# Kernel tuning notes

Hardware: AMD Instinct MI355X
Metric: run time of the kernel (lower is better)

Reference implementation:

```python
import jax, jax.numpy as jnp
import numpy as np

N = 1000; K = 500; M = N - K          # codeword / info / parity bits
NUE = 4; NBS = 4                      # tx / rx antennas
BPS = 4; RATE = 0.5; NSYM = N // BPS  # 16-QAM, 250 symbols per codeword
NITER = 5                             # BP iterations

# 16-QAM constellation, Gray-coded per axis (Sionna-style), unit energy
_bits = ((np.arange(16)[:, None] >> np.array([3, 2, 1, 0])) & 1).astype(np.float32)
_re = (1 - 2 * _bits[:, 0]) * (2 - (1 - 2 * _bits[:, 2]))
_im = (1 - 2 * _bits[:, 1]) * (2 - (1 - 2 * _bits[:, 3]))
POINTS = jnp.asarray((_re + 1j * _im) / np.sqrt(10.0), dtype=jnp.complex64)  # [16]
LABELS = jnp.asarray(_bits)  # [16,4] bit labels per point


def setup_inputs() -> dict:
    key = jax.random.key(0)
    ks = jax.random.split(key, 5)
    batch = 1000
    # systematic sparse LDPC-like code: H = [P^T | I_M], info-bit degree 3
    rs = np.random.RandomState(0)
    P = np.zeros((K, M), np.int32)
    for i in range(K):
        P[i, rs.choice(M, 3, replace=False)] = 1
    vi, ci = np.nonzero(P)
    vn = np.concatenate([vi, K + np.arange(M)]).astype(np.int32)  # [2000]
    cn = np.concatenate([ci, np.arange(M)]).astype(np.int32)      # [2000]
    b = jax.random.randint(ks[0], (batch, NUE, K), 0, 2, dtype=jnp.int32)
    h_re = jax.random.normal(ks[1], (batch * NSYM, NBS, NUE), jnp.float32)
    h_im = jax.random.normal(ks[2], (batch * NSYM, NBS, NUE), jnp.float32)
    n_re = jax.random.normal(ks[3], (batch * NSYM, NBS), jnp.float32)
    n_im = jax.random.normal(ks[4], (batch * NSYM, NBS), jnp.float32)
    return {"batch_size": batch, "ebno_db": jnp.full((1,), 5.0, jnp.float32),
            "b": b, "P": jnp.asarray(P), "cn_idx": jnp.asarray(cn),
            "vn_idx": jnp.asarray(vn), "h_re": h_re, "h_im": h_im,
            "noise_re": n_re, "noise_im": n_im}


def _forward(batch_size, ebno_db, b, P, cn_idx, vn_idx, h_re, h_im, noise_re, noise_im):
    no = 1.0 / (10.0 ** (ebno_db[0] / 10.0) * BPS * RATE)  # ebnodb2no
    # --- LDPC encode (systematic): c = [b, b@P mod 2] ---
    bf = b.astype(jnp.float32)
    parity = jnp.mod(jnp.round(bf @ P.astype(jnp.float32)), 2.0)
    c = jnp.concatenate([bf, parity], -1)                    # [B,NUE,N]
    # --- QAM mapper ---
    idx = (c.reshape(batch_size, NUE, NSYM, BPS) @ jnp.array([8., 4., 2., 1.], jnp.float32)).astype(jnp.int32)
    x = POINTS[idx]                                          # [B,NUE,NSYM]
    x_f = jnp.transpose(x, (0, 2, 1)).reshape(-1, NUE)       # [B*NSYM,NUE]
    # --- flat fading channel, h ~ CN(0,1), AWGN ---
    h = ((h_re + 1j * h_im) / np.sqrt(2.0)).astype(jnp.complex64)
    w = ((noise_re + 1j * noise_im) * jnp.sqrt(no / 2.0)).astype(jnp.complex64)
    y = jnp.einsum('bij,bj->bi', h, x_f) + w                 # [B*NSYM,NBS]
    # --- LMMSE equalizer: G = H^H (H H^H + no I)^-1, unbiased scaling ---
    A = jnp.einsum('bik,bjk->bij', h, jnp.conj(h)) \
        + no.astype(jnp.complex64) * jnp.eye(NBS, dtype=jnp.complex64)
    Ainv_y = jnp.linalg.solve(A, y[..., None])[..., 0]
    x_raw = jnp.einsum('bij,bi->bj', jnp.conj(h), Ainv_y)    # G y, [B*NSYM,NUE]
    GH = jnp.einsum('bij,bik->bjk', jnp.conj(h), jnp.linalg.solve(A, h))
    d = jnp.real(jnp.diagonal(GH, axis1=1, axis2=2))         # diag(GH), [B*NSYM,NUE]
    x_hat = x_raw / d.astype(jnp.complex64)
    no_eff = jnp.maximum(1.0 / d - 1.0, 1e-12)
    x_hat = jnp.transpose(x_hat.reshape(batch_size, NSYM, NUE), (0, 2, 1))  # [B,NUE,NSYM]
    nvar = jnp.transpose(no_eff.reshape(batch_size, NSYM, NUE), (0, 2, 1))
    # --- max-log demapper, L = log p(b=0)/p(b=1) ---
    metric = -(jnp.abs(x_hat[..., None] - POINTS) ** 2) / nvar[..., None]   # [B,NUE,NSYM,16]
    NEG = jnp.float32(-1e30)
    m5 = metric[..., None, :]                               # [B,NUE,NSYM,1,16]
    lab = LABELS.T[None, None, None]                        # [1,1,1,4,16]
    m0 = jnp.max(jnp.where(lab == 0, m5, NEG), -1)
    m1 = jnp.max(jnp.where(lab == 1, m5, NEG), -1)
    llr = (m0 - m1).reshape(batch_size, NUE, N)
    # --- LDPC BP decoder (sum-product over fixed sparse Tanner graph) ---
    Lch = llr.reshape(batch_size * NUE, N).T                # [N, Bc]
    c2v = jnp.zeros((cn_idx.shape[0], Lch.shape[1]), jnp.float32)  # [E, Bc]
    for _ in range(NITER):
        vtot = Lch.at[vn_idx].add(c2v)                      # Lch + segment_sum(c2v)
        m_vc = vtot[vn_idx] - c2v                           # extrinsic VN->CN
        t = jnp.tanh(jnp.clip(m_vc * 0.5, -9.9, 9.9))
        t = jnp.where(t >= 0, jnp.maximum(t, 1e-7), jnp.minimum(t, -1e-7))
        prod = jax.ops.segment_prod(t, cn_idx, num_segments=M)
        c2v = 2.0 * jnp.arctanh(jnp.clip(prod[cn_idx] / t, -0.999999, 0.999999))
    vtot = Lch.at[vn_idx].add(c2v)
    b_hat = (vtot[:K].T < 0).astype(jnp.float32).reshape(batch_size, NUE, K)
    return bf, b_hat


def reference(batch_size, ebno_db, b, P, cn_idx, vn_idx, h_re, h_im, noise_re, noise_im):
    return _forward(batch_size, ebno_db, b, P, cn_idx, vn_idx,
                    h_re, h_im, noise_re, noise_im)
```

## Files before the change

kernel.cpp:

```cpp
#include <hip/hip_runtime.h>
#include <math.h>

#define KK     500
#define MM     500
#define NNODES 1000
#define NSYM   250
#define NITERS 5
#define MAXVDEG 4
#define EMAX   2048
#define TB     256

#define SWZ(s) ((s) ^ (((s) >> 4) & 3))

__global__ void __launch_bounds__(512)
k_setup(const int* __restrict__ cn, const int* __restrict__ vn, int E,
        const float* __restrict__ ebno, const int* __restrict__ P,
        const int* __restrict__ b, int ncw,
        int* __restrict__ cinfo, int* __restrict__ vlist, int* __restrict__ coff,
        int* __restrict__ cdend, int* __restrict__ cperm,
        double* __restrict__ nobuf, unsigned* __restrict__ Ppack,
        unsigned* __restrict__ bpack, float* __restrict__ out, int packBlocks) {
  __shared__ int sdeg[512];
  __shared__ int scinv[512];
  __shared__ int sdnew[512];
  __shared__ int sexcl[512];
  __shared__ int ssc[512];
  __shared__ int scur[512];
  __shared__ int svc[NNODES];
  __shared__ int shist[64];
  __shared__ int shcur[64];
  int tid = threadIdx.x;
  int bx = blockIdx.x;

  if (bx == 0) {
    sdeg[tid] = 0;
    for (int n = tid; n < NNODES; n += 512) svc[n] = 0;
    if (tid < 64) { shist[tid] = 0; shcur[tid] = 0; }
    __syncthreads();
    for (int e = tid; e < E; e += 512) atomicAdd(&sdeg[cn[e]], 1);
    __syncthreads();
    int d = (tid < MM) ? sdeg[tid] : 0;
    if (tid < MM) atomicAdd(&shist[d], 1);
    __syncthreads();
    if (tid == 0) {
      int acc = 0;
      for (int i = 0; i < 64; ++i) { int h = shist[i]; shist[i] = acc; shcur[i] = acc; acc += h; }
    }
    __syncthreads();
    if (tid < MM) {
      int nid = atomicAdd(&shcur[d], 1);
      scinv[tid] = nid;
      cperm[nid] = tid;
      sdnew[nid] = d;
    }
    __syncthreads();
    int v = (tid < MM) ? sdnew[tid] : 0;
    ssc[tid] = v;
    __syncthreads();
    for (int o = 1; o < 512; o <<= 1) {
      int x = (tid >= o) ? ssc[tid - o] : 0;
      __syncthreads();
      ssc[tid] += x;
      __syncthreads();
    }
    int excl = ssc[tid] - v;
    sexcl[tid] = excl;
    scur[tid] = excl;
    if (tid < MM) {
      coff[tid]  = excl;
      cdend[tid] = excl + sdnew[tid] - 1;
      if (tid == MM - 1) coff[MM] = ssc[tid];
    }
    __syncthreads();
    for (int e = tid; e < E; e += 512) {
      int c = cn[e], n = vn[e];
      int nc = scinv[c];
      int slot;
      if (n >= KK) {
        slot = sexcl[nc] + sdeg[c] - 1;
      } else {
        slot = atomicAdd(&scur[nc], 1);
      }
      cinfo[slot] = (nc << 16) | n;
      if (n < KK) {
        int t = atomicAdd(&svc[n], 1);
        if (t < MAXVDEG) vlist[n * MAXVDEG + t] = slot;
      }
    }
    if (tid == 0) {
      double no = 1.0 / (pow(10.0, (double)ebno[0] * 0.1) * 2.0);
      nobuf[0] = no;
      nobuf[1] = sqrt(no * 0.5);
    }
    return;
  }

  if (bx <= packBlocks) {
    int id = (bx - 1) * 512 + tid;
    if (id < MM * 16) {
      int j = id >> 4, w = id & 15;
      unsigned word = 0u;
      int base = w * 32;
      for (int bit = 0; bit < 32; ++bit) {
        int i = base + bit;
        if (i < KK && P[i * MM + j] != 0) word |= (1u << bit);
      }
      Ppack[j * 16 + w] = word;
    } else {
      int id2 = id - MM * 16;
      if (id2 < ncw * 16) {
        int cw = id2 >> 4, w = id2 & 15;
        unsigned word = 0u;
        int base = w * 32;
        for (int bit = 0; bit < 32; ++bit) {
          int i = base + bit;
          if (i < KK && b[cw * KK + i] != 0) word |= (1u << bit);
        }
        bpack[cw * 16 + w] = word;
      }
    }
    return;
  }

  int id = (bx - 1 - packBlocks) * 512 + tid;
  if (id < ncw * KK) out[id] = (float)b[id];
}

__device__ __forceinline__ void qam_pointf(int p, float& re, float& im) {
  const float s = 0.31622776601683794f;
  int b0 = (p >> 3) & 1, b1 = (p >> 2) & 1, b2 = (p >> 1) & 1, b3 = p & 1;
  re = (float)((1 - 2 * b0) * (2 - (1 - 2 * b2))) * s;
  im = (float)((1 - 2 * b1) * (2 - (1 - 2 * b3))) * s;
}

__device__ __forceinline__ float tanh_half(float m) {
  float mc = fminf(fmaxf(m, -19.8f), 19.8f);
  float e = __expf(mc);
  float t = 1.0f - __fdividef(2.0f, e + 1.0f);
  return (t >= 0.0f) ? fmaxf(t, 1e-7f) : fminf(t, -1e-7f);
}
__device__ __forceinline__ float pclip(float P, float t) {
  return copysignf(fminf(fabsf(P), 0.999999f * fabsf(t)), P);
}
__device__ __forceinline__ float tfloor(float t) {
  return (t >= 0.0f) ? fmaxf(t, 1e-7f) : fminf(t, -1e-7f);
}
__device__ __forceinline__ float atanh2c(float P, float t) {
  float r = __fdividef(P, t);
  r = fminf(fmaxf(r, -0.999999f), 0.999999f);
  return __logf(__fdividef(1.0f + r, 1.0f - r));
}

#define SOLVE_DEMAP(J, Lout) {                                                          \
  float u0r = Hr[0][J] * i00,               u0i = Hi[0][J] * i00;                       \
  float u1r = (Hr[1][J] - (L10r * u0r - L10i * u0i)) * i11;                             \
  float u1i = (Hi[1][J] - (L10r * u0i + L10i * u0r)) * i11;                             \
  float u2r = (Hr[2][J] - (L20r * u0r - L20i * u0i) - (L21r * u1r - L21i * u1i)) * i22; \
  float u2i = (Hi[2][J] - (L20r * u0i + L20i * u0r) - (L21r * u1i + L21i * u1r)) * i22; \
  float u3r = (Hr[3][J] - (L30r * u0r - L30i * u0i) - (L31r * u1r - L31i * u1i)         \
                        - (L32r * u2r - L32i * u2i)) * i33;                             \
  float u3i = (Hi[3][J] - (L30r * u0i + L30i * u0r) - (L31r * u1i + L31i * u1r)         \
                        - (L32r * u2i + L32i * u2r)) * i33;                             \
  float dj = (u0r * u0r + u0i * u0i) + (u1r * u1r + u1i * u1i)                          \
           + (u2r * u2r + u2i * u2i) + (u3r * u3r + u3i * u3i);                         \
  float rr = (u0r * yr[0] + u0i * yi[0]) + (u1r * yr[1] + u1i * yi[1])                  \
           + (u2r * yr[2] + u2i * yi[2]) + (u3r * yr[3] + u3i * yi[3]);                 \
  float ri = (u0r * yi[0] - u0i * yr[0]) + (u1r * yi[1] - u1i * yr[1])                  \
           + (u2r * yi[2] - u2i * yr[2]) + (u3r * yi[3] - u3i * yr[3]);                 \
  float rdj = __fdividef(1.0f, dj);                                                    \
  float xhr = rr * rdj, xhi = ri * rdj;                                                \
  float gap = 1.0f - dj;                                                               \
  float inoe = __fdividef(dj, fmaxf(gap, dj * 1e-12f));                                \
  float m0[4] = {-1e30f, -1e30f, -1e30f, -1e30f};                                      \
  float m1[4] = {-1e30f, -1e30f, -1e30f, -1e30f};                                      \
  _Pragma("unroll")                                                                    \
  for (int p = 0; p < 16; ++p) {                                                       \
    float dr = xhr - PRT[p], di = xhi - PIT[p];                                        \
    float met = -(dr * dr + di * di) * inoe;                                           \
    _Pragma("unroll")                                                                  \
    for (int k = 0; k < 4; ++k) {                                                      \
      if ((p >> (3 - k)) & 1) m1[k] = fmaxf(m1[k], met);                               \
      else                    m0[k] = fmaxf(m0[k], met);                               \
    }                                                                                  \
  }                                                                                    \
  _Pragma("unroll")                                                                    \
  for (int k = 0; k < 4; ++k) Lout[k] = m0[k] - m1[k];                                 \
}

__global__ void __launch_bounds__(256, 4)
k_fused(const float* __restrict__ h_re, const float* __restrict__ h_im,
        const float* __restrict__ n_re, const float* __restrict__ n_im,
        const double* __restrict__ nobuf,
        const unsigned* __restrict__ bpack, const unsigned* __restrict__ Ppack,
        const int* __restrict__ vlist, const int* __restrict__ coff,
        const int* __restrict__ cdend, const int* __restrict__ cperm,
        const int* __restrict__ cinfo, float* __restrict__ out, int ncw) {
  __shared__ float2 sT[EMAX];
  __shared__ float2 sP[512];
  float2* sL = sT;

  int tid = threadIdx.x;
  int pairId = blockIdx.x;
  int bt = pairId >> 1, plane = pairId & 1;

  if (tid < NSYM) {
    int t = bt * NSYM + tid;
    int s = tid;

    float no = (float)nobuf[0];
    float sq = (float)nobuf[1];
    const float is2 = 0.70710678118654752f;

    float Hr[4][4], Hi[4][4];
    {
      const float4* hr4 = (const float4*)h_re;
      const float4* hi4 = (const float4*)h_im;
      #pragma unroll
      for (int i = 0; i < 4; ++i) {
        float4 a = hr4[t * 4 + i], c = hi4[t * 4 + i];
        Hr[i][0] = a.x * is2; Hr[i][1] = a.y * is2;
        Hr[i][2] = a.z * is2; Hr[i][3] = a.w * is2;
        Hi[i][0] = c.x * is2; Hi[i][1] = c.y * is2;
        Hi[i][2] = c.z * is2; Hi[i][3] = c.w * is2;
      }
    }

    float xr[4], xi[4];
    #pragma unroll
    for (int ue = 0; ue < 4; ++ue) {
      const unsigned* bp = bpack + (bt * 4 + ue) * 16;
      int v = 0;
      #pragma unroll
      for (int k = 0; k < 4; ++k) {
        int n = 4 * s + k;
        int bit;
        if (n < KK) {
          bit = (bp[n >> 5] >> (n & 31)) & 1;
        } else {
          const unsigned* pp = Ppack + (n - KK) * 16;
          int cnt = 0;
          #pragma unroll
          for (int w = 0; w < 16; ++w) cnt += __popc(bp[w] & pp[w]);
          bit = cnt & 1;
        }
        v = (v << 1) | bit;
      }
      qam_pointf(v, xr[ue], xi[ue]);
    }

    float yr[4], yi[4];
    {
      float4 wr = ((const float4*)n_re)[t];
      float4 wi = ((const float4*)n_im)[t];
      float wrv[4] = {wr.x, wr.y, wr.z, wr.w};
      float wiv[4] = {wi.x, wi.y, wi.z, wi.w};
      #pragma unroll
      for (int i = 0; i < 4; ++i) {
        float ar = wrv[i] * sq;
        float ai = wiv[i] * sq;
        #pragma unroll
        for (int j = 0; j < 4; ++j) {
          ar += Hr[i][j] * xr[j] - Hi[i][j] * xi[j];
          ai += Hr[i][j] * xi[j] + Hi[i][j] * xr[j];
        }
        yr[i] = ar; yi[i] = ai;
      }
    }

    auto dotc = [&](int i, int j, float& ar, float& ai) {
      float r = 0.0f, m = 0.0f;
      #pragma unroll
      for (int k = 0; k < 4; ++k) {
        r += Hr[i][k] * Hr[j][k] + Hi[i][k] * Hi[j][k];
        m += Hi[i][k] * Hr[j][k] - Hr[i][k] * Hi[j][k];
      }
      ar = r; ai = m;
    };
    float a00, a11, a22, a33, dum;
    float a10r, a10i, a20r, a20i, a21r, a21i, a30r, a30i, a31r, a31i, a32r, a32i;
    dotc(0, 0, a00, dum);  a00 += no;
    dotc(1, 0, a10r, a10i);
    dotc(1, 1, a11, dum);  a11 += no;
    dotc(2, 0, a20r, a20i);
    dotc(2, 1, a21r, a21i);
    dotc(2, 2, a22, dum);  a22 += no;
    dotc(3, 0, a30r, a30i);
    dotc(3, 1, a31r, a31i);
    dotc(3, 2, a32r, a32i);
    dotc(3, 3, a33, dum);  a33 += no;

    float i00 = rsqrtf(a00);
    float L10r = a10r * i00, L10i = a10i * i00;
    float L20r = a20r * i00, L20i = a20i * i00;
    float L30r = a30r * i00, L30i = a30i * i00;
    float d11 = a11 - (L10r * L10r + L10i * L10i);
    float i11 = rsqrtf(d11);
    float L21r = (a21r - (L20r * L10r + L20i * L10i)) * i11;
    float L21i = (a21i - (L20i * L10r - L20r * L10i)) * i11;
    float L31r = (a31r - (L30r * L10r + L30i * L10i)) * i11;
    float L31i = (a31i - (L30i * L10r - L30r * L10i)) * i11;
    float d22 = a22 - (L20r * L20r + L20i * L20i) - (L21r * L21r + L21i * L21i);
    float i22 = rsqrtf(d22);
    float L32r = (a32r - (L30r * L20r + L30i * L20i) - (L31r * L21r + L31i * L21i)) * i22;
    float L32i = (a32i - (L30i * L20r - L30r * L20i) - (L31i * L21r - L31r * L21i)) * i22;
    float d33 = a33 - (L30r * L30r + L30i * L30i) - (L31r * L31r + L31i * L31i)
                    - (L32r * L32r + L32i * L32i);
    float i33 = rsqrtf(d33);

    {
      float v0r = yr[0] * i00,               v0i = yi[0] * i00;
      float v1r = (yr[1] - (L10r * v0r - L10i * v0i)) * i11;
      float v1i = (yi[1] - (L10r * v0i + L10i * v0r)) * i11;
      float v2r = (yr[2] - (L20r * v0r - L20i * v0i) - (L21r * v1r - L21i * v1i)) * i22;
      float v2i = (yi[2] - (L20r * v0i + L20i * v0r) - (L21r * v1i + L21i * v1r)) * i22;
      float v3r = (yr[3] - (L30r * v0r - L30i * v0i) - (L31r * v1r - L31i * v1i)
                         - (L32r * v2r - L32i * v2i)) * i33;
      float v3i = (yi[3] - (L30r * v0i + L30i * v0r) - (L31r * v1i + L31i * v1r)
                         - (L32r * v2i + L32i * v2r)) * i33;
      yr[0] = v0r; yi[0] = v0i; yr[1] = v1r; yi[1] = v1i;
      yr[2] = v2r; yi[2] = v2i; yr[3] = v3r; yi[3] = v3i;
    }

    const float PRT[16] = { 0.31622776601683794f, 0.31622776601683794f, 0.9486832980505138f, 0.9486832980505138f,
                            0.31622776601683794f, 0.31622776601683794f, 0.9486832980505138f, 0.9486832980505138f,
                           -0.31622776601683794f,-0.31622776601683794f,-0.9486832980505138f,-0.9486832980505138f,
                           -0.31622776601683794f,-0.31622776601683794f,-0.9486832980505138f,-0.9486832980505138f };
    const float PIT[16] = { 0.31622776601683794f, 0.9486832980505138f, 0.31622776601683794f, 0.9486832980505138f,
                           -0.31622776601683794f,-0.9486832980505138f,-0.31622776601683794f,-0.9486832980505138f,
                            0.31622776601683794f, 0.9486832980505138f, 0.31622776601683794f, 0.9486832980505138f,
                           -0.31622776601683794f,-0.9486832980505138f,-0.31622776601683794f,-0.9486832980505138f };

    float lA[4], lB[4];
    if (plane == 0) {
      SOLVE_DEMAP(0, lA);
      SOLVE_DEMAP(1, lB);
    } else {
      SOLVE_DEMAP(2, lA);
      SOLVE_DEMAP(3, lB);
    }
    #pragma unroll
    for (int k = 0; k < 4; ++k) {
      sL[4 * s + k] = make_float2(lA[k], lB[k]);
    }
  }
  __syncthreads();

  float2 Ln[2], En[2];
  int pk0[2], pk1[2], pk2[2]; bool iok[2];
  #pragma unroll
  for (int i = 0; i < 2; ++i) {
    int n = tid + TB * i;
    iok[i] = n < KK;
    Ln[i] = make_float2(0.f, 0.f);
    En[i] = make_float2(1.f, 1.f);
    pk0[i] = pk1[i] = pk2[i] = 0;
    if (iok[i]) {
      float2 L = sL[n];
      Ln[i] = L;
      En[i] = make_float2(__expf(fminf(fmaxf(L.x, -55.f), 55.f)),
                          __expf(fminf(fmaxf(L.y, -55.f), 55.f)));
      int s0 = vlist[n * MAXVDEG], s1 = vlist[n * MAXVDEG + 1], s2 = vlist[n * MAXVDEG + 2];
      pk0[i] = (cinfo[s0] & 0xffff0000) | SWZ(s0);
      pk1[i] = (cinfo[s1] & 0xffff0000) | SWZ(s1);
      pk2[i] = (cinfo[s2] & 0xffff0000) | SWZ(s2);
    }
  }
  float2 qpar0, qpar1;
  {
    int oc0 = cperm[tid];
    float2 Lp0 = sL[KK + oc0];
    qpar0 = make_float2(tanh_half(Lp0.x), tanh_half(Lp0.y));
  }
  bool c1ok = (tid + TB) < MM;
  if (c1ok) {
    int oc1 = cperm[tid + TB];
    float2 Lp1 = sL[KK + oc1];
    qpar1 = make_float2(tanh_half(Lp1.x), tanh_half(Lp1.y));
  } else {
    qpar1 = make_float2(1.f, 1.f);
  }
  int beg0 = coff[tid],                  dnd0 = cdend[tid];
  int beg1 = c1ok ? coff[tid + TB]  : 0, dnd1 = c1ok ? cdend[tid + TB] : 0;
  __syncthreads();

  for (int it = 0; it < NITERS; ++it) {
    if (it == 0) {
      #pragma unroll
      for (int i = 0; i < 2; ++i) {
        if (iok[i]) {
          float2 t = make_float2(tanh_half(Ln[i].x), tanh_half(Ln[i].y));
          sT[pk0[i] & 0xffff] = t;
          sT[pk1[i] & 0xffff] = t;
          sT[pk2[i] & 0xffff] = t;
        }
      }
    } else {
      #pragma unroll
      for (int i = 0; i < 2; ++i) {
        if (iok[i]) {
          int s0 = pk0[i] & 0xffff, c0 = ((unsigned)pk0[i]) >> 16;
          int s1 = pk1[i] & 0xffff, c1 = ((unsigned)pk1[i]) >> 16;
          int s2 = pk2[i] & 0xffff, c2 = ((unsigned)pk2[i]) >> 16;
          float2 P0 = sP[c0], P1 = sP[c1], P2 = sP[c2];
          float2 t0 = sT[s0], t1 = sT[s1], t2 = sT[s2];
          float p0 = pclip(P0.x, t0.x), p1 = pclip(P1.x, t1.x), p2 = pclip(P2.x, t2.x);
          float a0 = t0.x + p0, a1 = t1.x + p1, a2 = t2.x + p2;
          float b0 = t0.x - p0, b1 = t1.x - p1, b2 = t2.x - p2;
          float Ex = En[i].x;
          float A0 = Ex * (a1 * a2), A1 = Ex * (a0 * a2), A2 = Ex * (a0 * a1);
          float B0 = b1 * b2,        B1 = b0 * b2,        B2 = b0 * b1;
          float n0x = tfloor(__fdividef(A0 - B0, A0 + B0));
          float n1x = tfloor(__fdividef(A1 - B1, A1 + B1));
          float n2x = tfloor(__fdividef(A2 - B2, A2 + B2));
          float q0 = pclip(P0.y, t0.y), q1 = pclip(P1.y, t1.y), q2 = pclip(P2.y, t2.y);
          float c0a = t0.y + q0, c1a = t1.y + q1, c2a = t2.y + q2;
          float d0b = t0.y - q0, d1b = t1.y - q1, d2b = t2.y - q2;
          float Ey = En[i].y;
          float C0 = Ey * (c1a * c2a), C1 = Ey * (c0a * c2a), C2 = Ey * (c0a * c1a);
          float D0 = d1b * d2b,        D1 = d0b * d2b,        D2 = d0b * d1b;
          float n0y = tfloor(__fdividef(C0 - D0, C0 + D0));
          float n1y = tfloor(__fdividef(C1 - D1, C1 + D1));
          float n2y = tfloor(__fdividef(C2 - D2, C2 + D2));
          sT[s0] = make_float2(n0x, n0y);
          sT[s1] = make_float2(n1x, n1y);
          sT[s2] = make_float2(n2x, n2y);
        }
      }
    }
    __syncthreads();
    {
      float px = qpar0.x, py = qpar0.y;
      for (int e = beg0; e < dnd0; ++e) { float2 tt = sT[SWZ(e)]; px *= tt.x; py *= tt.y; }
      sP[tid] = make_float2(px, py);
      if (c1ok) {
        float qx = qpar1.x, qy = qpar1.y;
        for (int e = beg1; e < dnd1; ++e) { float2 tt = sT[SWZ(e)]; qx *= tt.x; qy *= tt.y; }
        sP[tid + TB] = make_float2(qx, qy);
      }
    }
    __syncthreads();
  }

  int cw0 = pairId * 2;
  float* o0 = out + (size_t)ncw * KK + (size_t)cw0 * KK;
  float* o1 = o0 + KK;
  #pragma unroll
  for (int i = 0; i < 2; ++i) {
    if (iok[i]) {
      int n = tid + TB * i;
      int s0 = pk0[i] & 0xffff, c0 = ((unsigned)pk0[i]) >> 16;
      int s1 = pk1[i] & 0xffff, c1 = ((unsigned)pk1[i]) >> 16;
      int s2 = pk2[i] & 0xffff, c2 = ((unsigned)pk2[i]) >> 16;
      float2 P0 = sP[c0], P1 = sP[c1], P2 = sP[c2];
      float2 t0 = sT[s0], t1 = sT[s1], t2 = sT[s2];
      float2 L = Ln[i];
      float ax = L.x + atanh2c(P0.x, t0.x) + atanh2c(P1.x, t1.x) + atanh2c(P2.x, t2.x);
      float ay = L.y + atanh2c(P0.y, t0.y) + atanh2c(P1.y, t1.y) + atanh2c(P2.y, t2.y);
      o0[n] = (ax < 0.0f) ? 1.0f : 0.0f;
      o1[n] = (ay < 0.0f) ? 1.0f : 0.0f;
    }
  }
}

extern "C" void kernel_launch(void* const* d_in, const int* in_sizes, int n_in,
                              void* d_out, int out_size, void* d_ws, size_t ws_size,
                              hipStream_t stream) {
  const float* ebno = (const float*)d_in[1];
  const int*   b    = (const int*)d_in[2];
  const int*   P    = (const int*)d_in[3];
  const int*   cn   = (const int*)d_in[4];
  const int*   vn   = (const int*)d_in[5];
  const float* h_re = (const float*)d_in[6];
  const float* h_im = (const float*)d_in[7];
  const float* nre  = (const float*)d_in[8];
  const float* nim  = (const float*)d_in[9];
  float* out = (float*)d_out;

  int E     = in_sizes[4];
  int batch = in_sizes[2] / (4 * KK);
  int ncw   = batch * 4;

  char* ws = (char*)d_ws;
  size_t off = 0;
  auto alloc = [&](size_t bytes) -> void* {
    void* p = ws + off;
    off += (bytes + 255) & ~(size_t)255;
    return p;
  };
  unsigned* Ppack  = (unsigned*)alloc((size_t)MM * 16 * 4);
  unsigned* bpack  = (unsigned*)alloc((size_t)ncw * 16 * 4);
  int*      coff   = (int*)alloc((size_t)(MM + 1) * 4);
  int*      cdend  = (int*)alloc((size_t)MM * 4);
  int*      cperm  = (int*)alloc((size_t)MM * 4);
  int*      cinfo  = (int*)alloc((size_t)EMAX * 4);
  int*      vlist  = (int*)alloc((size_t)NNODES * MAXVDEG * 4);
  double*   nobuf  = (double*)alloc(2 * 8);
  (void)ws_size; (void)n_in; (void)out_size;

  int packItems  = MM * 16 + ncw * 16;
  int packBlocks = (packItems + 511) / 512;
  int bfBlocks   = (ncw * KK + 511) / 512;
  int setupGrid  = 1 + packBlocks + bfBlocks;

  k_setup<<<dim3(setupGrid), dim3(512), 0, stream>>>(cn, vn, E, ebno, P, b, ncw,
                                                     cinfo, vlist, coff, cdend, cperm,
                                                     nobuf, Ppack, bpack, out, packBlocks);
  k_fused<<<dim3(ncw / 2), dim3(256), 0, stream>>>(h_re, h_im, nre, nim, nobuf,
                                                   bpack, Ppack, vlist, coff, cdend,
                                                   cperm, cinfo, out, ncw);
}
```

Measured before the change: 176.8 us.

## Decode all four user codewords per block instead of two

Each block now handles one batch item with all four UE codewords, vectorised as float4 in shared memory, instead of two blocks each handling two codewords. This removes the duplicated channel loading, Cholesky factorisation and index/packing work that both half-blocks previously repeated. In exchange the grid is halved, and shared memory per block and register pressure (float4 state, four demaps per thread) roughly double, which may reduce occupancy.

```diff
diff --git a/kernel.cpp b/kernel.cpp
--- a/kernel.cpp
+++ b/kernel.cpp
@@ -138,6 +138,9 @@
   float e = __expf(mc);
   float t = 1.0f - __fdividef(2.0f, e + 1.0f);
   return (t >= 0.0f) ? fmaxf(t, 1e-7f) : fminf(t, -1e-7f);
+}
+__device__ __forceinline__ float4 tanh_half4(float4 m) {
+  return make_float4(tanh_half(m.x), tanh_half(m.y), tanh_half(m.z), tanh_half(m.w));
 }
 __device__ __forceinline__ float pclip(float P, float t) {
   return copysignf(fminf(fabsf(P), 0.999999f * fabsf(t)), P);
@@ -187,6 +190,18 @@
   for (int k = 0; k < 4; ++k) Lout[k] = m0[k] - m1[k];                                 \
 }
 
+#define VUPD(C) {                                                                      \
+  float p0 = pclip(P0.C, t0.C), p1 = pclip(P1.C, t1.C), p2 = pclip(P2.C, t2.C);        \
+  float a0 = t0.C + p0, a1 = t1.C + p1, a2 = t2.C + p2;                                \
+  float b0 = t0.C - p0, b1 = t1.C - p1, b2 = t2.C - p2;                                \
+  float Ec = En[i].C;                                                                  \
+  float A0 = Ec * (a1 * a2), A1 = Ec * (a0 * a2), A2 = Ec * (a0 * a1);                 \
+  float B0 = b1 * b2,        B1 = b0 * b2,        B2 = b0 * b1;                        \
+  n0.C = tfloor(__fdividef(A0 - B0, A0 + B0));                                         \
+  n1.C = tfloor(__fdividef(A1 - B1, A1 + B1));                                         \
+  n2.C = tfloor(__fdividef(A2 - B2, A2 + B2));                                         \
+}
+
 __global__ void __launch_bounds__(256, 4)
 k_fused(const float* __restrict__ h_re, const float* __restrict__ h_im,
         const float* __restrict__ n_re, const float* __restrict__ n_im,
@@ -195,13 +210,12 @@
         const int* __restrict__ vlist, const int* __restrict__ coff,
         const int* __restrict__ cdend, const int* __restrict__ cperm,
         const int* __restrict__ cinfo, float* __restrict__ out, int ncw) {
-  __shared__ float2 sT[EMAX];
-  __shared__ float2 sP[512];
-  float2* sL = sT;
+  __shared__ float4 sT[EMAX];
+  __shared__ float4 sP[512];
+  float4* sL = sT;
 
   int tid = threadIdx.x;
-  int pairId = blockIdx.x;
-  int bt = pairId >> 1, plane = pairId & 1;
+  int bt = blockIdx.x;
 
   if (tid < NSYM) {
     int t = bt * NSYM + tid;
@@ -330,54 +344,51 @@
                             0.31622776601683794f, 0.9486832980505138f, 0.31622776601683794f, 0.9486832980505138f,
                            -0.31622776601683794f,-0.9486832980505138f,-0.31622776601683794f,-0.9486832980505138f };
 
-    float lA[4], lB[4];
-    if (plane == 0) {
-      SOLVE_DEMAP(0, lA);
-      SOLVE_DEMAP(1, lB);
-    } else {
-      SOLVE_DEMAP(2, lA);
-      SOLVE_DEMAP(3, lB);
-    }
+    float l0[4], l1[4], l2[4], l3[4];
+    SOLVE_DEMAP(0, l0);
+    SOLVE_DEMAP(1, l1);
+    SOLVE_DEMAP(2, l2);
+    SOLVE_DEMAP(3, l3);
     #pragma unroll
     for (int k = 0; k < 4; ++k) {
-      sL[4 * s + k] = make_float2(lA[k], lB[k]);
+      sL[4 * s + k] = make_float4(l0[k], l1[k], l2[k], l3[k]);
     }
   }
   __syncthreads();
 
-  float2 Ln[2], En[2];
+  float4 Ln[2], En[2];
   int pk0[2], pk1[2], pk2[2]; bool iok[2];
   #pragma unroll
   for (int i = 0; i < 2; ++i) {
     int n = tid + TB * i;
     iok[i] = n < KK;
-    Ln[i] = make_float2(0.f, 0.f);
-    En[i] = make_float2(1.f, 1.f);
+    Ln[i] = make_float4(0.f, 0.f, 0.f, 0.f);
+    En[i] = make_float4(1.f, 1.f, 1.f, 1.f);
     pk0[i] = pk1[i] = pk2[i] = 0;
     if (iok[i]) {
-      float2 L = sL[n];
+      float4 L = sL[n];
       Ln[i] = L;
-      En[i] = make_float2(__expf(fminf(fmaxf(L.x, -55.f), 55.f)),
-                          __expf(fminf(fmaxf(L.y, -55.f), 55.f)));
+      En[i] = make_float4(__expf(fminf(fmaxf(L.x, -55.f), 55.f)),
+                          __expf(fminf(fmaxf(L.y, -55.f), 55.f)),
+                          __expf(fminf(fmaxf(L.z, -55.f), 55.f)),
+                          __expf(fminf(fmaxf(L.w, -55.f), 55.f)));
       int s0 = vlist[n * MAXVDEG], s1 = vlist[n * MAXVDEG + 1], s2 = vlist[n * MAXVDEG + 2];
       pk0[i] = (cinfo[s0] & 0xffff0000) | SWZ(s0);
       pk1[i] = (cinfo[s1] & 0xffff0000) | SWZ(s1);
       pk2[i] = (cinfo[s2] & 0xffff0000) | SWZ(s2);
     }
   }
-  float2 qpar0, qpar1;
+  float4 qpar0, qpar1;
   {
     int oc0 = cperm[tid];
-    float2 Lp0 = sL[KK + oc0];
-    qpar0 = make_float2(tanh_half(Lp0.x), tanh_half(Lp0.y));
+    qpar0 = tanh_half4(sL[KK + oc0]);
   }
   bool c1ok = (tid + TB) < MM;
   if (c1ok) {
     int oc1 = cperm[tid + TB];
-    float2 Lp1 = sL[KK + oc1];
-    qpar1 = make_float2(tanh_half(Lp1.x), tanh_half(Lp1.y));
+    qpar1 = tanh_half4(sL[KK + oc1]);
   } else {
-    qpar1 = make_float2(1.f, 1.f);
+    qpar1 = make_float4(1.f, 1.f, 1.f, 1.f);
   }
   int beg0 = coff[tid],                  dnd0 = cdend[tid];
   int beg1 = c1ok ? coff[tid + TB]  : 0, dnd1 = c1ok ? cdend[tid + TB] : 0;
@@ -388,7 +399,7 @@
       #pragma unroll
       for (int i = 0; i < 2; ++i) {
         if (iok[i]) {
-          float2 t = make_float2(tanh_half(Ln[i].x), tanh_half(Ln[i].y));
+          float4 t = tanh_half4(Ln[i]);
           sT[pk0[i] & 0xffff] = t;
           sT[pk1[i] & 0xffff] = t;
           sT[pk2[i] & 0xffff] = t;
@@ -401,49 +412,41 @@
           int s0 = pk0[i] & 0xffff, c0 = ((unsigned)pk0[i]) >> 16;
           int s1 = pk1[i] & 0xffff, c1 = ((unsigned)pk1[i]) >> 16;
           int s2 = pk2[i] & 0xffff, c2 = ((unsigned)pk2[i]) >> 16;
-          float2 P0 = sP[c0], P1 = sP[c1], P2 = sP[c2];
-          float2 t0 = sT[s0], t1 = sT[s1], t2 = sT[s2];
-          float p0 = pclip(P0.x, t0.x), p1 = pclip(P1.x, t1.x), p2 = pclip(P2.x, t2.x);
-          float a0 = t0.x + p0, a1 = t1.x + p1, a2 = t2.x + p2;
-          float b0 = t0.x - p0, b1 = t1.x - p1, b2 = t2.x - p2;
-          float Ex = En[i].x;
-          float A0 = Ex * (a1 * a2), A1 = Ex * (a0 * a2), A2 = Ex * (a0 * a1);
-          float B0 = b1 * b2,        B1 = b0 * b2,        B2 = b0 * b1;
-          float n0x = tfloor(__fdividef(A0 - B0, A0 + B0));
-          float n1x = tfloor(__fdividef(A1 - B1, A1 + B1));
-          float n2x = tfloor(__fdividef(A2 - B2, A2 + B2));
-          float q0 = pclip(P0.y, t0.y), q1 = pclip(P1.y, t1.y), q2 = pclip(P2.y, t2.y);
-          float c0a = t0.y + q0, c1a = t1.y + q1, c2a = t2.y + q2;
-          float d0b = t0.y - q0, d1b = t1.y - q1, d2b = t2.y - q2;
-          float Ey = En[i].y;
-          float C0 = Ey * (c1a * c2a), C1 = Ey * (c0a * c2a), C2 = Ey * (c0a * c1a);
-          float D0 = d1b * d2b,        D1 = d0b * d2b,        D2 = d0b * d1b;
-          float n0y = tfloor(__fdividef(C0 - D0, C0 + D0));
-          float n1y = tfloor(__fdividef(C1 - D1, C1 + D1));
-          float n2y = tfloor(__fdividef(C2 - D2, C2 + D2));
-          sT[s0] = make_float2(n0x, n0y);
-          sT[s1] = make_float2(n1x, n1y);
-          sT[s2] = make_float2(n2x, n2y);
+          float4 P0 = sP[c0], P1 = sP[c1], P2 = sP[c2];
+          float4 t0 = sT[s0], t1 = sT[s1], t2 = sT[s2];
+          float4 n0, n1, n2;
+          VUPD(x); VUPD(y); VUPD(z); VUPD(w);
+          sT[s0] = n0;
+          sT[s1] = n1;
+          sT[s2] = n2;
         }
       }
     }
     __syncthreads();
     {
-      float px = qpar0.x, py = qpar0.y;
-      for (int e = beg0; e < dnd0; ++e) { float2 tt = sT[SWZ(e)]; px *= tt.x; py *= tt.y; }
-      sP[tid] = make_float2(px, py);
+      float4 p = qpar0;
+      for (int e = beg0; e < dnd0; ++e) {
+        float4 tt = sT[SWZ(e)];
+        p.x *= tt.x; p.y *= tt.y; p.z *= tt.z; p.w *= tt.w;
+      }
+      sP[tid] = p;
       if (c1ok) {
-        float qx = qpar1.x, qy = qpar1.y;
-        for (int e = beg1; e < dnd1; ++e) { float2 tt = sT[SWZ(e)]; qx *= tt.x; qy *= tt.y; }
-        sP[tid + TB] = make_float2(qx, qy);
-      }
-    }
-    __syncthreads();
-  }
-
-  int cw0 = pairId * 2;
+        float4 q = qpar1;
+        for (int e = beg1; e < dnd1; ++e) {
+          float4 tt = sT[SWZ(e)];
+          q.x *= tt.x; q.y *= tt.y; q.z *= tt.z; q.w *= tt.w;
+        }
+        sP[tid + TB] = q;
+      }
+    }
+    __syncthreads();
+  }
+
+  int cw0 = bt * 4;
   float* o0 = out + (size_t)ncw * KK + (size_t)cw0 * KK;
   float* o1 = o0 + KK;
+  float* o2 = o1 + KK;
+  float* o3 = o2 + KK;
   #pragma unroll
   for (int i = 0; i < 2; ++i) {
     if (iok[i]) {
@@ -451,13 +454,17 @@
       int s0 = pk0[i] & 0xffff, c0 = ((unsigned)pk0[i]) >> 16;
       int s1 = pk1[i] & 0xffff, c1 = ((unsigned)pk1[i]) >> 16;
       int s2 = pk2[i] & 0xffff, c2 = ((unsigned)pk2[i]) >> 16;
-      float2 P0 = sP[c0], P1 = sP[c1], P2 = sP[c2];
-      float2 t0 = sT[s0], t1 = sT[s1], t2 = sT[s2];
-      float2 L = Ln[i];
+      float4 P0 = sP[c0], P1 = sP[c1], P2 = sP[c2];
+      float4 t0 = sT[s0], t1 = sT[s1], t2 = sT[s2];
+      float4 L = Ln[i];
       float ax = L.x + atanh2c(P0.x, t0.x) + atanh2c(P1.x, t1.x) + atanh2c(P2.x, t2.x);
       float ay = L.y + atanh2c(P0.y, t0.y) + atanh2c(P1.y, t1.y) + atanh2c(P2.y, t2.y);
+      float az = L.z + atanh2c(P0.z, t0.z) + atanh2c(P1.z, t1.z) + atanh2c(P2.z, t2.z);
+      float aw = L.w + atanh2c(P0.w, t0.w) + atanh2c(P1.w, t1.w) + atanh2c(P2.w, t2.w);
       o0[n] = (ax < 0.0f) ? 1.0f : 0.0f;
       o1[n] = (ay < 0.0f) ? 1.0f : 0.0f;
+      o2[n] = (az < 0.0f) ? 1.0f : 0.0f;
+      o3[n] = (aw < 0.0f) ? 1.0f : 0.0f;
     }
   }
 }
@@ -505,7 +512,7 @@
   k_setup<<<dim3(setupGrid), dim3(512), 0, stream>>>(cn, vn, E, ebno, P, b, ncw,
                                                      cinfo, vlist, coff, cdend, cperm,
                                                      nobuf, Ppack, bpack, out, packBlocks);
-  k_fused<<<dim3(ncw / 2), dim3(256), 0, stream>>>(h_re, h_im, nre, nim, nobuf,
-                                                   bpack, Ppack, vlist, coff, cdend,
-                                                   cperm, cinfo, out, ncw);
-}
+  k_fused<<<dim3(batch), dim3(256), 0, stream>>>(h_re, h_im, nre, nim, nobuf,
+                                                 bpack, Ppack, vlist, coff, cdend,
+                                                 cperm, cinfo, out, ncw);
+}
```

After: 169.3 us. -4.3%, faster.
